# Kernel optimization log

Hardware: AMD Instinct MI355X
Metric: run time of the kernel (lower is better)

Reference implementation:

```python
import jax, jax.numpy as jnp
import numpy as np

H, W_GRID = 64, 64          # grid size -> N = 4096 stations
CTX, HID = 512, 2048        # ctx_features, hidden_size
K, BATCH = 8, 8             # nearest_k, batch
N = H * W_GRID


def _build_neighbors(seed=0):
    """Mimics __init__: for each grid cell, k nearest cells by Euclidean grid
    distance, with similarity exp(-||f_i - f_j||) from a random scalar field."""
    rng = np.random.default_rng(seed)
    field = rng.standard_normal((H, W_GRID)).astype(np.float32)
    ii, jj = np.meshgrid(np.arange(H), np.arange(W_GRID), indexing='ij')
    coords = np.stack([ii.ravel(), jj.ravel()], axis=1).astype(np.float32)  # [N,2]
    d2 = ((coords[:, None, :] - coords[None, :, :]) ** 2).sum(-1).astype(np.float32)
    np.fill_diagonal(d2, np.inf)                      # exclude self (m!=i or n!=j)
    nn_idx = np.argsort(d2, axis=1)[:, :K].astype(np.int32)   # [N,K] flat ids
    f = field.ravel()
    sim = np.exp(-np.abs(f[:, None] - f[nn_idx])).astype(np.float32)  # [N,K]
    return nn_idx, sim


def setup_inputs() -> dict:
    key = jax.random.key(0)
    k1, k2 = jax.random.split(key)
    contextual_val = jax.random.normal(k1, (BATCH, H, W_GRID, CTX), dtype=jnp.float32)
    W = jax.random.normal(k2, (CTX, HID), dtype=jnp.float32)
    nn_idx, sim = _build_neighbors(seed=0)
    return {
        "contextual_val": contextual_val,
        "W": W,
        "nn_idx": jnp.asarray(nn_idx),
        "sim": jnp.asarray(sim),
    }


def reference(contextual_val, W, nn_idx, sim):
    # res[b, n, :] = sum_k sim[n, k] * (x[b, nn_idx[n, k], :] @ W)
    # By linearity: aggregate neighbor features with similarity weights first,
    # then apply the shared projection W once (same math, one GEMM).
    B = contextual_val.shape[0]
    x = contextual_val.reshape(B, N, CTX)          # [B, N, C]
    gathered = x[:, nn_idx]                        # [B, N, K, C] neighbor gather
    agg = jnp.einsum('nk,bnkc->bnc', sim, gathered)  # weighted scatter-add
    out = jnp.einsum('bnc,ch->bnh', agg, W)          # shared small matmul
    return out.reshape(B, H, W_GRID, HID)
```

## Files before the change

### kernel.cpp

```cpp
#include <hip/hip_runtime.h>
#include <cstdint>

#define CTX 512
#define HID 2048
#define NCELL 4096
#define M_TOT 32768

typedef __bf16 bf16;
typedef __attribute__((ext_vector_type(8))) __bf16 bf16x8;
typedef __attribute__((ext_vector_type(4))) float f32x4;

__device__ __align__(16) unsigned short g_agg[(size_t)M_TOT * CTX];
__device__ __align__(16) unsigned short g_WT[(size_t)HID * CTX];
__device__ int g_flag;

__device__ __forceinline__ float bf2f(unsigned short u) {
  union { unsigned int i; float f; } c; c.i = ((unsigned int)u) << 16; return c.f;
}
__device__ __forceinline__ unsigned short f2bf(float f) {
  union { float f; unsigned int i; } c; c.f = f;
  unsigned int u = c.i;
  u += 0x7fffu + ((u >> 16) & 1u);
  return (unsigned short)(u >> 16);
}
__device__ __forceinline__ float lo16(unsigned int w) {
  union { unsigned int i; float f; } c; c.i = w << 16; return c.f;
}
__device__ __forceinline__ float hi16(unsigned int w) {
  union { unsigned int i; float f; } c; c.i = w & 0xffff0000u; return c.f;
}

__device__ __forceinline__ void gload_lds16(const void* g, void* s) {
  __builtin_amdgcn_global_load_lds(
      (const __attribute__((address_space(1))) void*)g,
      (__attribute__((address_space(3))) void*)s, 16, 0, 0);
}

__global__ void detect_dtype(const unsigned short* __restrict__ x, int* flagp) {
  __shared__ int cnt;
  if (threadIdx.x == 0) cnt = 0;
  __syncthreads();
  const uint4 v = ((const uint4*)x)[threadIdx.x];
  unsigned int w[4] = {v.x, v.y, v.z, v.w};
  int c = 0;
#pragma unroll
  for (int i = 0; i < 4; ++i) {
    unsigned int lo = w[i] & 0xffffu, hi = w[i] >> 16;
    c += (((lo >> 7) & 0xffu) >= 0xF8u);
    c += (((hi >> 7) & 0xffu) >= 0xF8u);
  }
  atomicAdd(&cnt, c);
  __syncthreads();
  if (threadIdx.x == 0) *flagp = (cnt > 8) ? 1 : 0;
}

__global__ void transpose_w(const void* __restrict__ Wv,
                            unsigned short* __restrict__ wt,
                            const int* __restrict__ flagp) {
  const int isf32 = *flagp;
  const int t  = threadIdx.x;
  const int h  = blockIdx.x * 64 + (t & 63);
  const int c0 = (blockIdx.y * 4 + (t >> 6)) * 8;
  float e[8];
  if (isf32) {
    const float* Wf = (const float*)Wv;
#pragma unroll
    for (int j = 0; j < 8; ++j) e[j] = Wf[(size_t)(c0 + j) * HID + h];
  } else {
    const unsigned short* Wb = (const unsigned short*)Wv;
#pragma unroll
    for (int j = 0; j < 8; ++j) e[j] = bf2f(Wb[(size_t)(c0 + j) * HID + h]);
  }
  uint4 o;
  o.x = (unsigned int)f2bf(e[0]) | ((unsigned int)f2bf(e[1]) << 16);
  o.y = (unsigned int)f2bf(e[2]) | ((unsigned int)f2bf(e[3]) << 16);
  o.z = (unsigned int)f2bf(e[4]) | ((unsigned int)f2bf(e[5]) << 16);
  o.w = (unsigned int)f2bf(e[6]) | ((unsigned int)f2bf(e[7]) << 16);
  *(uint4*)&wt[(size_t)h * CTX + c0] = o;
}

__global__ void gather_agg_k(const void* __restrict__ xv,
                             const int* __restrict__ nn_idx,
                             const void* __restrict__ simv,
                             unsigned short* __restrict__ agg,
                             const int* __restrict__ flagp) {
  const int isf32 = *flagp;
  const int bid  = blockIdx.x;
  const int sb   = (bid & 7) * 1024 + (bid >> 3);
  const int m    = sb * 4 + (threadIdx.x >> 6);
  const int lane = threadIdx.x & 63;
  const int b    = m >> 12;
  const int n    = m & (NCELL - 1);
  const int c0   = lane * 8;

  float a[8] = {0, 0, 0, 0, 0, 0, 0, 0};
  if (isf32) {
    const float* xf = (const float*)xv;
    const float* sf = (const float*)simv;
#pragma unroll
    for (int k = 0; k < 8; ++k) {
      const int   idx = nn_idx[n * 8 + k];
      const float wgt = sf[n * 8 + k];
      const float* p  = xf + ((size_t)(b * NCELL + idx) * CTX + c0);
      const float4 v0 = *(const float4*)p;
      const float4 v1 = *(const float4*)(p + 4);
      a[0] += wgt * v0.x; a[1] += wgt * v0.y; a[2] += wgt * v0.z; a[3] += wgt * v0.w;
      a[4] += wgt * v1.x; a[5] += wgt * v1.y; a[6] += wgt * v1.z; a[7] += wgt * v1.w;
    }
  } else {
    const unsigned short* xb = (const unsigned short*)xv;
    const unsigned short* sb16 = (const unsigned short*)simv;
#pragma unroll
    for (int k = 0; k < 8; ++k) {
      const int   idx = nn_idx[n * 8 + k];
      const float wgt = bf2f(sb16[n * 8 + k]);
      const uint4 v = *(const uint4*)(xb + ((size_t)(b * NCELL + idx) * CTX + c0));
      a[0] += wgt * lo16(v.x); a[1] += wgt * hi16(v.x);
      a[2] += wgt * lo16(v.y); a[3] += wgt * hi16(v.y);
      a[4] += wgt * lo16(v.z); a[5] += wgt * hi16(v.z);
      a[6] += wgt * lo16(v.w); a[7] += wgt * hi16(v.w);
    }
  }
  uint4 o;
  o.x = (unsigned int)f2bf(a[0]) | ((unsigned int)f2bf(a[1]) << 16);
  o.y = (unsigned int)f2bf(a[2]) | ((unsigned int)f2bf(a[3]) << 16);
  o.z = (unsigned int)f2bf(a[4]) | ((unsigned int)f2bf(a[5]) << 16);
  o.w = (unsigned int)f2bf(a[6]) | ((unsigned int)f2bf(a[7]) << 16);
  *(uint4*)&agg[(size_t)m * CTX + c0] = o;
}

#define CS_STR 132
__global__ __launch_bounds__(256) void gemm_bt(const unsigned short* __restrict__ agg,
                                               const unsigned short* __restrict__ wt,
                                               void* __restrict__ outv,
                                               const int* __restrict__ flagp) {
  __shared__ __align__(16) char smem[33792];
  bf16*  As = (bf16*)smem;
  bf16*  Bs = (bf16*)(smem + 16384);
  float* Cs = (float*)smem;

  const int tid  = threadIdx.x;
  const int wave = tid >> 6;
  const int lane = tid & 63;
  const int l16  = lane & 15;
  const int quad = lane >> 4;

  const int bid = blockIdx.x;
  const int swz = (bid & 7) * 512 + (bid >> 3);
  const int gn0 = (swz & 15) * 128;
  const int gm0 = (swz >> 4) * 128;

  const int wm = (wave & 1) * 64;
  const int wn = (wave >> 1) * 64;

  f32x4 acc[4][4] = {};

  const int srow = lane >> 3;
  const int scol = (lane & 7) * 8;

  for (int kt = 0; kt < CTX; kt += 64) {
#pragma unroll
    for (int i = 0; i < 4; ++i) {
      const int chunk = wave * 4 + i;
      const int row   = chunk * 8 + srow;
      gload_lds16(&agg[(size_t)(gm0 + row) * CTX + kt + scol], &As[chunk * 512]);
      gload_lds16(&wt [(size_t)(gn0 + row) * CTX + kt + scol], &Bs[chunk * 512]);
    }
    __syncthreads();
#pragma unroll
    for (int s = 0; s < 2; ++s) {
      bf16x8 af[4], bfr[4];
#pragma unroll
      for (int mi = 0; mi < 4; ++mi)
        af[mi] = *(const bf16x8*)&As[(wm + mi * 16 + l16) * 64 + (s * 4 + quad) * 8];
#pragma unroll
      for (int ni = 0; ni < 4; ++ni)
        bfr[ni] = *(const bf16x8*)&Bs[(wn + ni * 16 + l16) * 64 + (s * 4 + quad) * 8];
#pragma unroll
      for (int mi = 0; mi < 4; ++mi)
#pragma unroll
        for (int ni = 0; ni < 4; ++ni)
          acc[mi][ni] = __builtin_amdgcn_mfma_f32_16x16x32_bf16(
              af[mi], bfr[ni], acc[mi][ni], 0, 0, 0);
    }
    __syncthreads();
  }

  const int isf32 = *flagp;
  if (isf32) {
    float* out = (float*)outv;
#pragma unroll
    for (int h = 0; h < 2; ++h) {
      __syncthreads();
      if ((wave & 1) == h) {
#pragma unroll
        for (int mi = 0; mi < 4; ++mi)
#pragma unroll
          for (int r = 0; r < 4; ++r) {
            const int lr = mi * 16 + quad * 4 + r;
#pragma unroll
            for (int ni = 0; ni < 4; ++ni)
              Cs[lr * CS_STR + wn + ni * 16 + l16] = acc[mi][ni][r];
          }
      }
      __syncthreads();
#pragma unroll
      for (int p = 0; p < 8; ++p) {
        const int r  = p * 8 + (tid >> 5);
        const int c4 = (tid & 31) * 4;
        const f32x4 v = *(const f32x4*)&Cs[r * CS_STR + c4];
        *(f32x4*)&out[(size_t)(gm0 + h * 64 + r) * HID + gn0 + c4] = v;
      }
    }
  } else {
    unsigned short* out = (unsigned short*)outv;
#pragma unroll
    for (int mi = 0; mi < 4; ++mi)
#pragma unroll
      for (int r = 0; r < 4; ++r) {
        const size_t row = (size_t)(gm0 + wm + mi * 16 + quad * 4 + r);
#pragma unroll
        for (int ni = 0; ni < 4; ++ni)
          out[row * HID + gn0 + wn + ni * 16 + l16] = f2bf(acc[mi][ni][r]);
      }
  }
}

extern "C" void kernel_launch(void* const* d_in, const int* in_sizes, int n_in,
                              void* d_out, int out_size, void* d_ws, size_t ws_size,
                              hipStream_t stream) {
  const void* x   = d_in[0];
  const void* W   = d_in[1];
  const int*  nn  = (const int*)d_in[2];
  const void* sim = d_in[3];

  const size_t wt_bytes  = (size_t)HID * CTX * 2;
  const size_t agg_bytes = (size_t)M_TOT * CTX * 2;
  const size_t need      = wt_bytes + agg_bytes + 16;

  unsigned short *wt, *agg; int* flagp;
  if (ws_size >= need) {
    wt    = (unsigned short*)d_ws;
    agg   = (unsigned short*)((char*)d_ws + wt_bytes);
    flagp = (int*)((char*)d_ws + wt_bytes + agg_bytes);
  } else {
    void *p0, *p1, *p2;
    hipGetSymbolAddress(&p0, HIP_SYMBOL(g_WT));
    hipGetSymbolAddress(&p1, HIP_SYMBOL(g_agg));
    hipGetSymbolAddress(&p2, HIP_SYMBOL(g_flag));
    wt = (unsigned short*)p0; agg = (unsigned short*)p1; flagp = (int*)p2;
  }

  detect_dtype<<<1, 256, 0, stream>>>((const unsigned short*)x, flagp);
  transpose_w<<<dim3(HID / 64, CTX / 32), 256, 0, stream>>>(W, wt, flagp);
  gather_agg_k<<<dim3(M_TOT / 4), 256, 0, stream>>>(x, nn, sim, agg, flagp);
  gemm_bt<<<dim3((HID / 128) * (M_TOT / 128)), 256, 0, stream>>>(agg, wt, d_out, flagp);
}
```

Before: 442.5 us.

## Double-buffer GEMM LDS tiles with XOR swizzle and coalesce fp32 gather loads

The GEMM main loop now double-buffers the A/B LDS tiles, issuing the next k-tile's global-to-LDS loads before computing on the current one, with explicit vmcnt waits and barriers. LDS columns are XOR-swizzled by row to cut bank conflicts, and s_setprio raises wave priority around the MFMA block. The fp32 gather path splits each lane's 8 channels into two contiguous halves so each float4 load across a wave is contiguous. This doubles LDS use to 64KB per block, which may lower occupancy, and relies on hand-counted vmcnt values being correct.

After: 405.6 us. 8.4% less time.

```diff
diff --git a/kernel.cpp b/kernel.cpp
--- a/kernel.cpp
+++ b/kernel.cpp
@@ -91,23 +91,32 @@
   const int lane = threadIdx.x & 63;
   const int b    = m >> 12;
   const int n    = m & (NCELL - 1);
-  const int c0   = lane * 8;
 
   float a[8] = {0, 0, 0, 0, 0, 0, 0, 0};
   if (isf32) {
+    const int clo = lane * 4;
+    const int chi = 256 + lane * 4;
     const float* xf = (const float*)xv;
     const float* sf = (const float*)simv;
 #pragma unroll
     for (int k = 0; k < 8; ++k) {
       const int   idx = nn_idx[n * 8 + k];
       const float wgt = sf[n * 8 + k];
-      const float* p  = xf + ((size_t)(b * NCELL + idx) * CTX + c0);
-      const float4 v0 = *(const float4*)p;
-      const float4 v1 = *(const float4*)(p + 4);
+      const float* p  = xf + (size_t)(b * NCELL + idx) * CTX;
+      const float4 v0 = *(const float4*)(p + clo);
+      const float4 v1 = *(const float4*)(p + chi);
       a[0] += wgt * v0.x; a[1] += wgt * v0.y; a[2] += wgt * v0.z; a[3] += wgt * v0.w;
       a[4] += wgt * v1.x; a[5] += wgt * v1.y; a[6] += wgt * v1.z; a[7] += wgt * v1.w;
     }
-  } else {
+    uint2 olo, ohi;
+    olo.x = (unsigned int)f2bf(a[0]) | ((unsigned int)f2bf(a[1]) << 16);
+    olo.y = (unsigned int)f2bf(a[2]) | ((unsigned int)f2bf(a[3]) << 16);
+    ohi.x = (unsigned int)f2bf(a[4]) | ((unsigned int)f2bf(a[5]) << 16);
+    ohi.y = (unsigned int)f2bf(a[6]) | ((unsigned int)f2bf(a[7]) << 16);
+    *(uint2*)&agg[(size_t)m * CTX + clo] = olo;
+    *(uint2*)&agg[(size_t)m * CTX + chi] = ohi;
+  } else {
+    const int c0 = lane * 8;
     const unsigned short* xb = (const unsigned short*)xv;
     const unsigned short* sb16 = (const unsigned short*)simv;
 #pragma unroll
@@ -120,13 +129,13 @@
       a[4] += wgt * lo16(v.z); a[5] += wgt * hi16(v.z);
       a[6] += wgt * lo16(v.w); a[7] += wgt * hi16(v.w);
     }
-  }
-  uint4 o;
-  o.x = (unsigned int)f2bf(a[0]) | ((unsigned int)f2bf(a[1]) << 16);
-  o.y = (unsigned int)f2bf(a[2]) | ((unsigned int)f2bf(a[3]) << 16);
-  o.z = (unsigned int)f2bf(a[4]) | ((unsigned int)f2bf(a[5]) << 16);
-  o.w = (unsigned int)f2bf(a[6]) | ((unsigned int)f2bf(a[7]) << 16);
-  *(uint4*)&agg[(size_t)m * CTX + c0] = o;
+    uint4 o;
+    o.x = (unsigned int)f2bf(a[0]) | ((unsigned int)f2bf(a[1]) << 16);
+    o.y = (unsigned int)f2bf(a[2]) | ((unsigned int)f2bf(a[3]) << 16);
+    o.z = (unsigned int)f2bf(a[4]) | ((unsigned int)f2bf(a[5]) << 16);
+    o.w = (unsigned int)f2bf(a[6]) | ((unsigned int)f2bf(a[7]) << 16);
+    *(uint4*)&agg[(size_t)m * CTX + c0] = o;
+  }
 }
 
 #define CS_STR 132
@@ -134,9 +143,7 @@
                                                const unsigned short* __restrict__ wt,
                                                void* __restrict__ outv,
                                                const int* __restrict__ flagp) {
-  __shared__ __align__(16) char smem[33792];
-  bf16*  As = (bf16*)smem;
-  bf16*  Bs = (bf16*)(smem + 16384);
+  __shared__ __align__(16) char smem[65536];
   float* Cs = (float*)smem;
 
   const int tid  = threadIdx.x;
@@ -156,35 +163,65 @@
   f32x4 acc[4][4] = {};
 
   const int srow = lane >> 3;
-  const int scol = (lane & 7) * 8;
-
-  for (int kt = 0; kt < CTX; kt += 64) {
-#pragma unroll
-    for (int i = 0; i < 4; ++i) {
-      const int chunk = wave * 4 + i;
-      const int row   = chunk * 8 + srow;
-      gload_lds16(&agg[(size_t)(gm0 + row) * CTX + kt + scol], &As[chunk * 512]);
-      gload_lds16(&wt [(size_t)(gn0 + row) * CTX + kt + scol], &Bs[chunk * 512]);
-    }
-    __syncthreads();
+  const int l8   = lane & 7;
+
+#define STAGE(b, kt)                                                          \
+  {                                                                           \
+    bf16* As_ = (bf16*)(smem + (b) * 32768);                                  \
+    bf16* Bs_ = (bf16*)(smem + (b) * 32768 + 16384);                          \
+    _Pragma("unroll")                                                         \
+    for (int i = 0; i < 4; ++i) {                                             \
+      const int chunk = wave * 4 + i;                                         \
+      const int row   = chunk * 8 + srow;                                     \
+      const int csw   = (l8 * 8) ^ ((row & 7) << 3);                          \
+      gload_lds16(&agg[(size_t)(gm0 + row) * CTX + (kt) + csw],               \
+                  &As_[chunk * 512]);                                         \
+      gload_lds16(&wt[(size_t)(gn0 + row) * CTX + (kt) + csw],                \
+                  &Bs_[chunk * 512]);                                         \
+    }                                                                         \
+  }
+
+  STAGE(0, 0);
+
+  for (int t = 0; t < 8; ++t) {
+    if (t < 7) {
+      STAGE((t + 1) & 1, (t + 1) * 64);
+      asm volatile("s_waitcnt vmcnt(8)" ::: "memory");
+    } else {
+      asm volatile("s_waitcnt vmcnt(0)" ::: "memory");
+    }
+    __builtin_amdgcn_s_barrier();
+    __builtin_amdgcn_sched_barrier(0);
+
+    const bf16* A = (const bf16*)(smem + (t & 1) * 32768);
+    const bf16* B = (const bf16*)(smem + (t & 1) * 32768 + 16384);
+
 #pragma unroll
     for (int s = 0; s < 2; ++s) {
       bf16x8 af[4], bfr[4];
 #pragma unroll
-      for (int mi = 0; mi < 4; ++mi)
-        af[mi] = *(const bf16x8*)&As[(wm + mi * 16 + l16) * 64 + (s * 4 + quad) * 8];
-#pragma unroll
-      for (int ni = 0; ni < 4; ++ni)
-        bfr[ni] = *(const bf16x8*)&Bs[(wn + ni * 16 + l16) * 64 + (s * 4 + quad) * 8];
+      for (int mi = 0; mi < 4; ++mi) {
+        const int r = wm + mi * 16 + l16;
+        af[mi] = *(const bf16x8*)&A[r * 64 + (((s * 4 + quad) * 8) ^ ((r & 7) << 3))];
+      }
+#pragma unroll
+      for (int ni = 0; ni < 4; ++ni) {
+        const int r = wn + ni * 16 + l16;
+        bfr[ni] = *(const bf16x8*)&B[r * 64 + (((s * 4 + quad) * 8) ^ ((r & 7) << 3))];
+      }
+      __builtin_amdgcn_s_setprio(1);
 #pragma unroll
       for (int mi = 0; mi < 4; ++mi)
 #pragma unroll
         for (int ni = 0; ni < 4; ++ni)
           acc[mi][ni] = __builtin_amdgcn_mfma_f32_16x16x32_bf16(
               af[mi], bfr[ni], acc[mi][ni], 0, 0, 0);
-    }
-    __syncthreads();
-  }
+      __builtin_amdgcn_s_setprio(0);
+    }
+    __builtin_amdgcn_s_barrier();
+    __builtin_amdgcn_sched_barrier(0);
+  }
+#undef STAGE
 
   const int isf32 = *flagp;
   if (isf32) {
```
